# Kernel optimization log

Measured on AMD Instinct MI355X. Metric: run time of the kernel, lower is better.

The kernel has to match this reference:

```python
import jax, jax.numpy as jnp
import numpy as np

N_VOCAB = 50257
N_EMBED = 300
N_HIDDEN = 256
N_OUTPUT = 1
BATCH = 256
SEQ_LEN = 512


def setup_inputs() -> dict:
    key = jax.random.key(0)
    k1, k2, k3, k4, k5, k6 = jax.random.split(key, 6)
    input_words = jax.random.randint(k1, (BATCH, SEQ_LEN), 0, N_VOCAB, dtype=jnp.int64 if jax.config.jax_enable_x64 else jnp.int32)
    emb_table = jax.random.normal(k2, (N_VOCAB, N_EMBED), dtype=jnp.float32)
    Wi = jax.random.normal(k3, (N_EMBED, N_HIDDEN), dtype=jnp.float32)
    Wh = jax.random.normal(k4, (N_HIDDEN, N_HIDDEN), dtype=jnp.float32)
    # nn.Linear default init: U(-1/sqrt(in), 1/sqrt(in))
    bound = 1.0 / np.sqrt(N_HIDDEN)
    fc_w = jax.random.uniform(k5, (N_HIDDEN, N_OUTPUT), minval=-bound, maxval=bound, dtype=jnp.float32)
    fc_b = jax.random.uniform(k6, (N_OUTPUT,), minval=-bound, maxval=bound, dtype=jnp.float32)
    return {"input_words": input_words, "emb_table": emb_table, "Wi": Wi, "Wh": Wh, "fc_w": fc_w, "fc_b": fc_b}


def reference(input_words, emb_table, Wi, Wh, fc_w, fc_b):
    # [B, S, E] -> [S, B, E] (module permutes to time-major)
    embedded = emb_table[input_words].transpose(1, 0, 2)
    h0 = jnp.zeros((input_words.shape[0], Wh.shape[0]), dtype=embedded.dtype)

    def step(h, x_t):
        # recurrence: h = sigmoid(x_t @ Wi + h @ Wh)
        h_new = jax.nn.sigmoid(x_t @ Wi + h @ Wh)
        return h_new, None

    hidden, _ = jax.lax.scan(step, h0, embedded)
    sig = jax.nn.sigmoid(hidden @ fc_w + fc_b)
    return (sig, hidden)
```

## Files before the change

kernel.cpp:

```cpp
#include <hip/hip_runtime.h>

#define S_LEN 512
#define BATCH 256
#define EMB   300
#define HID   256
#define VOCAB 50257
#define NPROD 786
#define NLOG2E -1.44269504089f

#define EW_BYTES 25731584ull
#define KPAD 320

typedef __attribute__((ext_vector_type(8))) _Float16 f16x8;
typedef __attribute__((ext_vector_type(4))) _Float16 f16x4;
typedef __attribute__((ext_vector_type(2))) __fp16   fp16v2;
typedef __attribute__((ext_vector_type(4))) float    f32x4;

__device__ __forceinline__ void block_sync_lds() {
    asm volatile("" ::: "memory");
    __builtin_amdgcn_s_waitcnt(0xC07F);
    __builtin_amdgcn_s_barrier();
    asm volatile("" ::: "memory");
}

__device__ __forceinline__ float sigmoid_scaled(float xs) {
    float e = __builtin_amdgcn_exp2f(xs);
    return __builtin_amdgcn_rcpf(1.0f + e);
}

__global__ __launch_bounds__(256)
void k_wprep(const float* __restrict__ Wi, _Float16* __restrict__ WiT) {
    const int k = blockIdx.x;
    const int n = threadIdx.x;
    _Float16 v = (_Float16)0.f;
    if (k < EMB) v = (_Float16)(Wi[k * HID + n] * NLOG2E);
    WiT[n * KPAD + k] = v;
}

__global__ __launch_bounds__(256, 3)
void k_embwi(const float* __restrict__ emb, const _Float16* __restrict__ WiT,
             _Float16* __restrict__ EW) {
    const int tid  = threadIdx.x;
    const int wv   = tid >> 6;
    const int lane = tid & 63;
    const int ln   = lane & 15;
    const int q    = lane >> 4;
    const int m0   = blockIdx.x * 64;

    const _Float16* wbn[4];
#pragma unroll
    for (int nt = 0; nt < 4; nt++)
        wbn[nt] = WiT + (wv * 64 + nt * 16 + ln) * KPAD + q * 8;

    const float* arow[4];
#pragma unroll
    for (int mt = 0; mt < 4; mt++) {
        int row = m0 + mt * 16 + ln; if (row >= VOCAB) row = VOCAB - 1;
        arow[mt] = emb + (long)row * EMB + q * 8;
    }

    auto load_af = [&](int kc, int mt) -> f16x8 {
        const float* p = arow[mt] + kc * 32;
        f16x8 v;
        if (kc < 9 || q == 0) {
            f32x4 a = *(const f32x4*)p;
            f32x4 b = *(const f32x4*)(p + 4);
#pragma unroll
            for (int r = 0; r < 4; r++) { v[r] = (_Float16)a[r]; v[4 + r] = (_Float16)b[r]; }
        } else if (q == 1) {
            f32x4 a = *(const f32x4*)p;
#pragma unroll
            for (int r = 0; r < 4; r++) { v[r] = (_Float16)a[r]; v[4 + r] = (_Float16)0.f; }
        } else {
#pragma unroll
            for (int r = 0; r < 8; r++) v[r] = (_Float16)0.f;
        }
        return v;
    };

    f32x4 acc[4][4];
#pragma unroll
    for (int mt = 0; mt < 4; mt++)
#pragma unroll
        for (int nt = 0; nt < 4; nt++)
            acc[mt][nt] = f32x4{0.f, 0.f, 0.f, 0.f};

#pragma unroll
    for (int kc = 0; kc < 10; kc++) {
        f16x8 af[4], bf[4];
#pragma unroll
        for (int mt = 0; mt < 4; mt++) af[mt] = load_af(kc, mt);
#pragma unroll
        for (int nt = 0; nt < 4; nt++) bf[nt] = *(const f16x8*)(wbn[nt] + kc * 32);
#pragma unroll
        for (int mt = 0; mt < 4; mt++)
#pragma unroll
            for (int nt = 0; nt < 4; nt++)
                acc[mt][nt] = __builtin_amdgcn_mfma_f32_16x16x32_f16(
                    af[mt], bf[nt], acc[mt][nt], 0, 0, 0);
    }

#pragma unroll
    for (int mt = 0; mt < 4; mt++)
#pragma unroll
        for (int nt = 0; nt < 4; nt++) {
            const int col = wv * 64 + nt * 16 + ln;
#pragma unroll
            for (int r = 0; r < 4; r++) {
                const int mm = m0 + mt * 16 + q * 4 + r;
                if (mm < VOCAB) EW[(long)mm * HID + col] = (_Float16)acc[mt][nt][r];
            }
        }
}

#define HSTR 272
#define HB8  (8 * HSTR)
#define WSTR 513

__global__ __launch_bounds__(512, 2)
void k_recur(const float* __restrict__ Wh, const _Float16* __restrict__ EW,
             const int* __restrict__ words,
             const float* __restrict__ fcw, const float* __restrict__ fcb,
             float* __restrict__ out) {
    __shared__ __attribute__((aligned(16))) _Float16 hbuf[2 * HB8];
    __shared__ float red[512];
    __shared__ int   wlds[8 * WSTR];

    const int tid  = threadIdx.x;
    const int wv   = tid >> 6;
    const int lane = tid & 63;
    const int ln   = lane & 15;
    const int lnn  = ln & 7;
    const int q    = lane >> 4;
    const int b0   = blockIdx.x * 8;

    f16x8 whf[8][2];
#pragma unroll
    for (int kc = 0; kc < 8; kc++) {
#pragma unroll
        for (int mt = 0; mt < 2; mt++) {
            const int j = wv * 32 + mt * 16 + ln;
            f16x8 u;
#pragma unroll
            for (int jj = 0; jj < 8; jj++)
                u[jj] = (_Float16)(Wh[(kc * 32 + q * 8 + jj) * HID + j] * NLOG2E);
            whf[kc][mt] = u;
        }
    }

#pragma unroll
    for (int i = tid; i < 8 * S_LEN; i += 512) {
        const int r = i >> 9, c = i & 511;
        wlds[r * WSTR + c] = words[(b0 + r) * S_LEN + c];
    }
    for (int i = tid; i < 2 * HB8; i += 512) hbuf[i] = (_Float16)0.f;
    __syncthreads();

    const int jbase = wv * 32 + q * 4;
    f16x4 abuf0[2], abuf1[2];
    {
        const int w0 = wlds[lnn * WSTR + 0];
        const int w1 = wlds[lnn * WSTR + 1];
        const _Float16* p0 = EW + ((long)w0 << 8) + jbase;
        const _Float16* p1 = EW + ((long)w1 << 8) + jbase;
#pragma unroll
        for (int mt = 0; mt < 2; mt++) abuf0[mt] = *(const f16x4*)(p0 + mt * 16);
#pragma unroll
        for (int mt = 0; mt < 2; mt++) abuf1[mt] = *(const f16x4*)(p1 + mt * 16);
    }

#define STEP(T, ABUF)                                                                   \
    {                                                                                   \
        const int tt = (T);                                                             \
        const _Float16* hr = hbuf + ((tt & 1) ? HB8 : 0);                               \
        _Float16*       hw = hbuf + ((tt & 1) ? 0 : HB8);                               \
        f16x8 hf[8];                                                                    \
        _Pragma("unroll")                                                               \
        for (int kc = 0; kc < 8; kc++)                                                  \
            hf[kc] = *(const f16x8*)(hr + lnn * HSTR + kc * 32 + q * 8);                \
        f32x4 acc_a[2], acc_b[2];                                                       \
        _Pragma("unroll")                                                               \
        for (int mt = 0; mt < 2; mt++) {               \
            f16x4 av = ABUF[mt];                                                        \
            acc_a[mt] = f32x4{(float)av[0], (float)av[1], (float)av[2], (float)av[3]};  \
            acc_b[mt] = f32x4{0.f, 0.f, 0.f, 0.f};                                      \
        }                                                                               \
        const int t2 = (tt + 2 > 511) ? 511 : (tt + 2);                                 \
        const int wrow = wlds[lnn * WSTR + t2];                                         \
        const _Float16* rp = EW + ((long)wrow << 8) + jbase;                            \
        _Pragma("unroll")                                                               \
        for (int mt = 0; mt < 2; mt++) ABUF[mt] = *(const f16x4*)(rp + mt * 16);        \
        _Pragma("unroll")                                                               \
        for (int r = 0; r < 4; r++) {                            \
            _Pragma("unroll")                                                           \
            for (int mt = 0; mt < 2; mt++)                                              \
                acc_a[mt] = __builtin_amdgcn_mfma_f32_16x16x32_f16(                     \
                    whf[r][mt], hf[r], acc_a[mt], 0, 0, 0);                             \
            _Pragma("unroll")                                                           \
            for (int mt = 0; mt < 2; mt++)                                              \
                acc_b[mt] = __builtin_amdgcn_mfma_f32_16x16x32_f16(                     \
                    whf[r + 4][mt], hf[r + 4], acc_b[mt], 0, 0, 0);                     \
        }                                                                               \
        _Pragma("unroll")                                                               \
        for (int mt = 0; mt < 2; mt++) {                                                \
            f32x4 s = acc_a[mt] + acc_b[mt];                                            \
            float r0 = sigmoid_scaled(s[0]), r1 = sigmoid_scaled(s[1]);                 \
            float r2 = sigmoid_scaled(s[2]), r3 = sigmoid_scaled(s[3]);                 \
            union { fp16v2 h2[2]; f16x4 v4; } hp;                                       \
            hp.h2[0] = __builtin_amdgcn_cvt_pkrtz(r0, r1);                              \
            hp.h2[1] = __builtin_amdgcn_cvt_pkrtz(r2, r3);                              \
            if (ln < 8)                                                                 \
                *(f16x4*)(hw + ln * HSTR + wv * 32 + mt * 16 + q * 4) = hp.v4;          \
        }                                                                               \
        block_sync_lds();                                                               \
    }

    for (int t = 0; t < S_LEN; t += 2) {
        STEP(t, abuf0);
        STEP(t + 1, abuf1);
    }
#undef STEP

    const _Float16* hf0 = hbuf;

    {
        const int row = tid >> 6, j0 = (tid & 63) * 4;
        float* dst = out + 256 + (long)(b0 + row) * HID + j0;
        f32x4 w;
#pragma unroll
        for (int r = 0; r < 4; r++) w[r] = (float)hf0[row * HSTR + j0 + r];
        *(f32x4*)dst = w;
    }

    {
        const int row = tid >> 6, part = tid & 63;
        float s = 0.f;
#pragma unroll
        for (int jj = 0; jj < 4; jj++) {
            const int j = part * 4 + jj;
            s += (float)hf0[row * HSTR + j] * fcw[j];
        }
        red[row * 64 + part] = s;
    }
    __syncthreads();
    if (tid < 8) {
        float s = fcb[0];
#pragma unroll
        for (int p = 0; p < 64; p++) s += red[tid * 64 + p];
        s *= NLOG2E;
        out[b0 + tid] = sigmoid_scaled(s);
    }
}

extern "C" void kernel_launch(void* const* d_in, const int* in_sizes, int n_in,
                              void* d_out, int out_size, void* d_ws, size_t ws_size,
                              hipStream_t stream) {
    const int*   words = (const int*)d_in[0];
    const float* emb   = (const float*)d_in[1];
    const float* Wi    = (const float*)d_in[2];
    const float* Wh    = (const float*)d_in[3];
    const float* fcw   = (const float*)d_in[4];
    const float* fcb   = (const float*)d_in[5];
    _Float16* EW   = (_Float16*)d_ws;
    _Float16* WiT  = (_Float16*)((char*)d_ws + EW_BYTES);
    float*    outp = (float*)d_out;

    hipLaunchKernelGGL(k_wprep, dim3(KPAD), dim3(256), 0, stream, Wi, WiT);
    hipLaunchKernelGGL(k_embwi, dim3(NPROD), dim3(256), 0, stream, emb, WiT, EW);
    hipLaunchKernelGGL(k_recur, dim3(BATCH / 8), dim3(512), 0, stream,
                       Wh, EW, words, fcw, fcb, outp);
}
```

Measured before the change: 419.0 us.

## Interleave two independent batch groups per block in the recurrence

Each recurrence block now handles 16 batch rows as two independent 8-row groups with separate hidden-state buffers. It alternates between them so that one group's LDS read of the hidden state overlaps the other group's MFMA and sigmoid work, hiding per-step latency in the serial chain. The grid is halved to 16 blocks and the launch bound drops to 1 block per SM. This trades parallelism across CUs for latency hiding within each block, and raises register and LDS pressure.

```diff
diff --git a/kernel.cpp b/kernel.cpp
--- a/kernel.cpp
+++ b/kernel.cpp
@@ -117,14 +117,15 @@
 #define HB8  (8 * HSTR)
 #define WSTR 513
 
-__global__ __launch_bounds__(512, 2)
+__global__ __launch_bounds__(512, 1)
 void k_recur(const float* __restrict__ Wh, const _Float16* __restrict__ EW,
              const int* __restrict__ words,
              const float* __restrict__ fcw, const float* __restrict__ fcb,
              float* __restrict__ out) {
-    __shared__ __attribute__((aligned(16))) _Float16 hbuf[2 * HB8];
+    __shared__ __attribute__((aligned(16))) _Float16 hbufA[2 * HB8];
+    __shared__ __attribute__((aligned(16))) _Float16 hbufB[2 * HB8];
     __shared__ float red[512];
-    __shared__ int   wlds[8 * WSTR];
+    __shared__ int   wlds[16 * WSTR];
 
     const int tid  = threadIdx.x;
     const int wv   = tid >> 6;
@@ -132,7 +133,7 @@
     const int ln   = lane & 15;
     const int lnn  = ln & 7;
     const int q    = lane >> 4;
-    const int b0   = blockIdx.x * 8;
+    const int b0   = blockIdx.x * 16;
 
     f16x8 whf[8][2];
 #pragma unroll
@@ -149,57 +150,60 @@
     }
 
 #pragma unroll
-    for (int i = tid; i < 8 * S_LEN; i += 512) {
+    for (int i = tid; i < 16 * S_LEN; i += 512) {
         const int r = i >> 9, c = i & 511;
         wlds[r * WSTR + c] = words[(b0 + r) * S_LEN + c];
     }
-    for (int i = tid; i < 2 * HB8; i += 512) hbuf[i] = (_Float16)0.f;
+    for (int i = tid; i < 2 * HB8; i += 512) { hbufA[i] = (_Float16)0.f; hbufB[i] = (_Float16)0.f; }
     __syncthreads();
 
     const int jbase = wv * 32 + q * 4;
-    f16x4 abuf0[2], abuf1[2];
+    const int* wrA = wlds + lnn * WSTR;
+    const int* wrB = wlds + (8 + lnn) * WSTR;
+
+    f16x4 abA0[2], abA1[2], abB0[2], abB1[2];
     {
-        const int w0 = wlds[lnn * WSTR + 0];
-        const int w1 = wlds[lnn * WSTR + 1];
-        const _Float16* p0 = EW + ((long)w0 << 8) + jbase;
-        const _Float16* p1 = EW + ((long)w1 << 8) + jbase;
-#pragma unroll
-        for (int mt = 0; mt < 2; mt++) abuf0[mt] = *(const f16x4*)(p0 + mt * 16);
-#pragma unroll
-        for (int mt = 0; mt < 2; mt++) abuf1[mt] = *(const f16x4*)(p1 + mt * 16);
-    }
-
-#define STEP(T, ABUF)                                                                   \
+        const _Float16* pA0 = EW + ((long)wrA[0] << 8) + jbase;
+        const _Float16* pA1 = EW + ((long)wrA[1] << 8) + jbase;
+        const _Float16* pB0 = EW + ((long)wrB[0] << 8) + jbase;
+        const _Float16* pB1 = EW + ((long)wrB[1] << 8) + jbase;
+#pragma unroll
+        for (int mt = 0; mt < 2; mt++) {
+            abA0[mt] = *(const f16x4*)(pA0 + mt * 16);
+            abA1[mt] = *(const f16x4*)(pA1 + mt * 16);
+            abB0[mt] = *(const f16x4*)(pB0 + mt * 16);
+            abB1[mt] = *(const f16x4*)(pB1 + mt * 16);
+        }
+    }
+
+#define READH(HF, HR)                                                                   \
+    _Pragma("unroll")                                                                   \
+    for (int kc = 0; kc < 8; kc++)                                                      \
+        HF[kc] = *(const f16x8*)((HR) + lnn * HSTR + kc * 32 + q * 8);
+
+#define GCOMP(HF, AB, HW, WR, T)                                                        \
     {                                                                                   \
-        const int tt = (T);                                                             \
-        const _Float16* hr = hbuf + ((tt & 1) ? HB8 : 0);                               \
-        _Float16*       hw = hbuf + ((tt & 1) ? 0 : HB8);                               \
-        f16x8 hf[8];                                                                    \
-        _Pragma("unroll")                                                               \
-        for (int kc = 0; kc < 8; kc++)                                                  \
-            hf[kc] = *(const f16x8*)(hr + lnn * HSTR + kc * 32 + q * 8);                \
         f32x4 acc_a[2], acc_b[2];                                                       \
         _Pragma("unroll")                                                               \
         for (int mt = 0; mt < 2; mt++) {               \
-            f16x4 av = ABUF[mt];                                                        \
+            f16x4 av = AB[mt];                                                          \
             acc_a[mt] = f32x4{(float)av[0], (float)av[1], (float)av[2], (float)av[3]};  \
             acc_b[mt] = f32x4{0.f, 0.f, 0.f, 0.f};                                      \
         }                                                                               \
-        const int t2 = (tt + 2 > 511) ? 511 : (tt + 2);                                 \
-        const int wrow = wlds[lnn * WSTR + t2];                                         \
-        const _Float16* rp = EW + ((long)wrow << 8) + jbase;                            \
-        _Pragma("unroll")                                                               \
-        for (int mt = 0; mt < 2; mt++) ABUF[mt] = *(const f16x4*)(rp + mt * 16);        \
+        const int t2_ = ((T) + 2 > 511) ? 511 : ((T) + 2);                              \
+        const _Float16* rp_ = EW + ((long)WR[t2_] << 8) + jbase;                        \
+        _Pragma("unroll")                                                               \
+        for (int mt = 0; mt < 2; mt++) AB[mt] = *(const f16x4*)(rp_ + mt * 16);         \
         _Pragma("unroll")                                                               \
         for (int r = 0; r < 4; r++) {                            \
             _Pragma("unroll")                                                           \
             for (int mt = 0; mt < 2; mt++)                                              \
                 acc_a[mt] = __builtin_amdgcn_mfma_f32_16x16x32_f16(                     \
-                    whf[r][mt], hf[r], acc_a[mt], 0, 0, 0);                             \
+                    whf[r][mt], HF[r], acc_a[mt], 0, 0, 0);                             \
             _Pragma("unroll")                                                           \
             for (int mt = 0; mt < 2; mt++)                                              \
                 acc_b[mt] = __builtin_amdgcn_mfma_f32_16x16x32_f16(                     \
-                    whf[r + 4][mt], hf[r + 4], acc_b[mt], 0, 0, 0);                     \
+                    whf[r + 4][mt], HF[r + 4], acc_b[mt], 0, 0, 0);                     \
         }                                                                               \
         _Pragma("unroll")                                                               \
         for (int mt = 0; mt < 2; mt++) {                                                \
@@ -210,43 +214,63 @@
             hp.h2[0] = __builtin_amdgcn_cvt_pkrtz(r0, r1);                              \
             hp.h2[1] = __builtin_amdgcn_cvt_pkrtz(r2, r3);                              \
             if (ln < 8)                                                                 \
-                *(f16x4*)(hw + ln * HSTR + wv * 32 + mt * 16 + q * 4) = hp.v4;          \
+                *(f16x4*)((HW) + ln * HSTR + wv * 32 + mt * 16 + q * 4) = hp.v4;        \
         }                                                                               \
+    }
+
+#define PHASE(T, ABA, ABB, HRB, HWA, HWB)                                               \
+    {                                                                                   \
+        READH(hfB, HRB);                                                                \
+        GCOMP(hfA, ABA, HWA, wrA, T);                                                   \
         block_sync_lds();                                                               \
-    }
+        READH(hfA, HWA);                                                                \
+        GCOMP(hfB, ABB, HWB, wrB, T);                                                   \
+        block_sync_lds();                                                               \
+    }
+
+    f16x8 hfA[8], hfB[8];
+    READH(hfA, hbufA);
 
     for (int t = 0; t < S_LEN; t += 2) {
-        STEP(t, abuf0);
-        STEP(t + 1, abuf1);
-    }
-#undef STEP
-
-    const _Float16* hf0 = hbuf;
+        PHASE(t,     abA0, abB0, hbufB,       hbufA + HB8, hbufB + HB8);
+        PHASE(t + 1, abA1, abB1, hbufB + HB8, hbufA,       hbufB);
+    }
+#undef PHASE
+#undef GCOMP
+#undef READH
 
     {
-        const int row = tid >> 6, j0 = (tid & 63) * 4;
+        const int row = tid >> 5, j0 = (tid & 31) * 8;
+        const _Float16* hsrc = (row < 8) ? (hbufA + row * HSTR)
+                                         : (hbufB + (row - 8) * HSTR);
         float* dst = out + 256 + (long)(b0 + row) * HID + j0;
-        f32x4 w;
-#pragma unroll
-        for (int r = 0; r < 4; r++) w[r] = (float)hf0[row * HSTR + j0 + r];
-        *(f32x4*)dst = w;
+        f32x4 w0v, w1v;
+#pragma unroll
+        for (int r = 0; r < 4; r++) {
+            w0v[r] = (float)hsrc[j0 + r];
+            w1v[r] = (float)hsrc[j0 + 4 + r];
+        }
+        *(f32x4*)dst = w0v;
+        *(f32x4*)(dst + 4) = w1v;
     }
 
     {
-        const int row = tid >> 6, part = tid & 63;
+        const int row = tid >> 5, part = tid & 31;
+        const _Float16* hsrc = (row < 8) ? (hbufA + row * HSTR)
+                                         : (hbufB + (row - 8) * HSTR);
         float s = 0.f;
 #pragma unroll
-        for (int jj = 0; jj < 4; jj++) {
-            const int j = part * 4 + jj;
-            s += (float)hf0[row * HSTR + j] * fcw[j];
-        }
-        red[row * 64 + part] = s;
+        for (int jj = 0; jj < 8; jj++) {
+            const int j = part * 8 + jj;
+            s += (float)hsrc[j] * fcw[j];
+        }
+        red[row * 32 + part] = s;
     }
     __syncthreads();
-    if (tid < 8) {
+    if (tid < 16) {
         float s = fcb[0];
 #pragma unroll
-        for (int p = 0; p < 64; p++) s += red[tid * 64 + p];
+        for (int p = 0; p < 32; p++) s += red[tid * 32 + p];
         s *= NLOG2E;
         out[b0 + tid] = sigmoid_scaled(s);
     }
@@ -267,6 +291,6 @@
 
     hipLaunchKernelGGL(k_wprep, dim3(KPAD), dim3(256), 0, stream, Wi, WiT);
     hipLaunchKernelGGL(k_embwi, dim3(NPROD), dim3(256), 0, stream, emb, WiT, EW);
-    hipLaunchKernelGGL(k_recur, dim3(BATCH / 8), dim3(512), 0, stream,
+    hipLaunchKernelGGL(k_recur, dim3(BATCH / 16), dim3(512), 0, stream,
                        Wh, EW, words, fcw, fcb, outp);
 }
```

New measurement: 659.0 us. +57.3%, slower.

## Split recurrence across more blocks with two batch rows each and four accumulator chains

Applied to the files above, without the earlier changes.

Each block now handles 2 batch rows instead of 8, so the recurrence kernel launches 128 blocks instead of 32 and uses more of the GPU's compute units. The MFMA chain is split into four independent accumulators so dependent MFMA latency can overlap. The cost is that most of each 16-wide MFMA tile is wasted on duplicated rows, and Wh is loaded into registers by four times as many blocks.

```diff
diff --git a/kernel.cpp b/kernel.cpp
--- a/kernel.cpp
+++ b/kernel.cpp
@@ -114,7 +114,8 @@
 }
 
 #define HSTR 272
-#define HB8  (8 * HSTR)
+#define NR   2
+#define HBR  (NR * HSTR)
 #define WSTR 513
 
 __global__ __launch_bounds__(512, 2)
@@ -122,17 +123,17 @@
              const int* __restrict__ words,
              const float* __restrict__ fcw, const float* __restrict__ fcb,
              float* __restrict__ out) {
-    __shared__ __attribute__((aligned(16))) _Float16 hbuf[2 * HB8];
-    __shared__ float red[512];
-    __shared__ int   wlds[8 * WSTR];
+    __shared__ __attribute__((aligned(16))) _Float16 hbuf[2 * HBR];
+    __shared__ float red[128];
+    __shared__ int   wlds[NR * WSTR];
 
     const int tid  = threadIdx.x;
     const int wv   = tid >> 6;
     const int lane = tid & 63;
     const int ln   = lane & 15;
-    const int lnn  = ln & 7;
+    const int lnn  = ln & (NR - 1);
     const int q    = lane >> 4;
-    const int b0   = blockIdx.x * 8;
+    const int b0   = blockIdx.x * NR;
 
     f16x8 whf[8][2];
 #pragma unroll
@@ -148,12 +149,11 @@
         }
     }
 
-#pragma unroll
-    for (int i = tid; i < 8 * S_LEN; i += 512) {
+    for (int i = tid; i < NR * S_LEN; i += 512) {
         const int r = i >> 9, c = i & 511;
         wlds[r * WSTR + c] = words[(b0 + r) * S_LEN + c];
     }
-    for (int i = tid; i < 2 * HB8; i += 512) hbuf[i] = (_Float16)0.f;
+    for (int i = tid; i < 2 * HBR; i += 512) hbuf[i] = (_Float16)0.f;
     __syncthreads();
 
     const int jbase = wv * 32 + q * 4;
@@ -172,18 +172,20 @@
 #define STEP(T, ABUF)                                                                   \
     {                                                                                   \
         const int tt = (T);                                                             \
-        const _Float16* hr = hbuf + ((tt & 1) ? HB8 : 0);                               \
-        _Float16*       hw = hbuf + ((tt & 1) ? 0 : HB8);                               \
+        const _Float16* hr = hbuf + ((tt & 1) ? HBR : 0);                               \
+        _Float16*       hw = hbuf + ((tt & 1) ? 0 : HBR);                               \
         f16x8 hf[8];                                                                    \
         _Pragma("unroll")                                                               \
         for (int kc = 0; kc < 8; kc++)                                                  \
             hf[kc] = *(const f16x8*)(hr + lnn * HSTR + kc * 32 + q * 8);                \
-        f32x4 acc_a[2], acc_b[2];                                                       \
+        f32x4 c0[2], c1[2], c2[2], c3[2];                                               \
         _Pragma("unroll")                                                               \
         for (int mt = 0; mt < 2; mt++) {               \
             f16x4 av = ABUF[mt];                                                        \
-            acc_a[mt] = f32x4{(float)av[0], (float)av[1], (float)av[2], (float)av[3]};  \
-            acc_b[mt] = f32x4{0.f, 0.f, 0.f, 0.f};                                      \
+            c0[mt] = f32x4{(float)av[0], (float)av[1], (float)av[2], (float)av[3]};     \
+            c1[mt] = f32x4{0.f, 0.f, 0.f, 0.f};                                         \
+            c2[mt] = f32x4{0.f, 0.f, 0.f, 0.f};                                         \
+            c3[mt] = f32x4{0.f, 0.f, 0.f, 0.f};                                         \
         }                                                                               \
         const int t2 = (tt + 2 > 511) ? 511 : (tt + 2);                                 \
         const int wrow = wlds[lnn * WSTR + t2];                                         \
@@ -191,26 +193,27 @@
         _Pragma("unroll")                                                               \
         for (int mt = 0; mt < 2; mt++) ABUF[mt] = *(const f16x4*)(rp + mt * 16);        \
         _Pragma("unroll")                                                               \
-        for (int r = 0; r < 4; r++) {                            \
+        for (int mt = 0; mt < 2; mt++) {                         \
+            c0[mt] = __builtin_amdgcn_mfma_f32_16x16x32_f16(whf[0][mt], hf[0], c0[mt], 0, 0, 0); \
+            c1[mt] = __builtin_amdgcn_mfma_f32_16x16x32_f16(whf[2][mt], hf[2], c1[mt], 0, 0, 0); \
+            c2[mt] = __builtin_amdgcn_mfma_f32_16x16x32_f16(whf[4][mt], hf[4], c2[mt], 0, 0, 0); \
+            c3[mt] = __builtin_amdgcn_mfma_f32_16x16x32_f16(whf[6][mt], hf[6], c3[mt], 0, 0, 0); \
+            c0[mt] = __builtin_amdgcn_mfma_f32_16x16x32_f16(whf[1][mt], hf[1], c0[mt], 0, 0, 0); \
+            c1[mt] = __builtin_amdgcn_mfma_f32_16x16x32_f16(whf[3][mt], hf[3], c1[mt], 0, 0, 0); \
+            c2[mt] = __builtin_amdgcn_mfma_f32_16x16x32_f16(whf[5][mt], hf[5], c2[mt], 0, 0, 0); \
+            c3[mt] = __builtin_amdgcn_mfma_f32_16x16x32_f16(whf[7][mt], hf[7], c3[mt], 0, 0, 0); \
+        }                                                                               \
+        if (ln < NR) {                                   \
             _Pragma("unroll")                                                           \
-            for (int mt = 0; mt < 2; mt++)                                              \
-                acc_a[mt] = __builtin_amdgcn_mfma_f32_16x16x32_f16(                     \
-                    whf[r][mt], hf[r], acc_a[mt], 0, 0, 0);                             \
-            _Pragma("unroll")                                                           \
-            for (int mt = 0; mt < 2; mt++)                                              \
-                acc_b[mt] = __builtin_amdgcn_mfma_f32_16x16x32_f16(                     \
-                    whf[r + 4][mt], hf[r + 4], acc_b[mt], 0, 0, 0);                     \
-        }                                                                               \
-        _Pragma("unroll")                                                               \
-        for (int mt = 0; mt < 2; mt++) {                                                \
-            f32x4 s = acc_a[mt] + acc_b[mt];                                            \
-            float r0 = sigmoid_scaled(s[0]), r1 = sigmoid_scaled(s[1]);                 \
-            float r2 = sigmoid_scaled(s[2]), r3 = sigmoid_scaled(s[3]);                 \
-            union { fp16v2 h2[2]; f16x4 v4; } hp;                                       \
-            hp.h2[0] = __builtin_amdgcn_cvt_pkrtz(r0, r1);                              \
-            hp.h2[1] = __builtin_amdgcn_cvt_pkrtz(r2, r3);                              \
-            if (ln < 8)                                                                 \
+            for (int mt = 0; mt < 2; mt++) {                                            \
+                f32x4 s = (c0[mt] + c1[mt]) + (c2[mt] + c3[mt]);                        \
+                float r0 = sigmoid_scaled(s[0]), r1 = sigmoid_scaled(s[1]);             \
+                float r2 = sigmoid_scaled(s[2]), r3 = sigmoid_scaled(s[3]);             \
+                union { fp16v2 h2[2]; f16x4 v4; } hp;                                   \
+                hp.h2[0] = __builtin_amdgcn_cvt_pkrtz(r0, r1);                          \
+                hp.h2[1] = __builtin_amdgcn_cvt_pkrtz(r2, r3);                          \
                 *(f16x4*)(hw + ln * HSTR + wv * 32 + mt * 16 + q * 4) = hp.v4;          \
+            }                                                                           \
         }                                                                               \
         block_sync_lds();                                                               \
     }
@@ -223,7 +226,7 @@
 
     const _Float16* hf0 = hbuf;
 
-    {
+    if (tid < 64 * NR) {
         const int row = tid >> 6, j0 = (tid & 63) * 4;
         float* dst = out + 256 + (long)(b0 + row) * HID + j0;
         f32x4 w;
@@ -232,7 +235,7 @@
         *(f32x4*)dst = w;
     }
 
-    {
+    if (tid < 64 * NR) {
         const int row = tid >> 6, part = tid & 63;
         float s = 0.f;
 #pragma unroll
@@ -243,7 +246,7 @@
         red[row * 64 + part] = s;
     }
     __syncthreads();
-    if (tid < 8) {
+    if (tid < NR) {
         float s = fcb[0];
 #pragma unroll
         for (int p = 0; p < 64; p++) s += red[tid * 64 + p];
@@ -267,6 +270,6 @@
 
     hipLaunchKernelGGL(k_wprep, dim3(KPAD), dim3(256), 0, stream, Wi, WiT);
     hipLaunchKernelGGL(k_embwi, dim3(NPROD), dim3(256), 0, stream, emb, WiT, EW);
-    hipLaunchKernelGGL(k_recur, dim3(BATCH / 8), dim3(512), 0, stream,
+    hipLaunchKernelGGL(k_recur, dim3(BATCH / NR), dim3(512), 0, stream,
                        Wh, EW, words, fcw, fcb, outp);
 }
```

Result: slower. 439.2 us (+4.8%).

## Permute EW columns for single 16-byte gather and drop split accumulators

Applied to the files above, without the earlier changes.

The projection kernel now writes EW with a permuted column order within each 32-column group. This lets each lane in the recurrence load its input contribution with one 8-half vector load per step instead of two 4-half loads. The recurrence uses two accumulators over all 8 k-chunks instead of four split ones. Lanes 8-15 take the second m-tile's result, so all 16 lanes do the sigmoid and store, which removes the masked half-idle epilogue. The last two steps are peeled so the clamp on the prefetch index no longer runs inside the loop. The trade-off is a longer dependent MFMA chain per accumulator in exchange for fewer adds and loads.

```diff
diff --git a/kernel.cpp b/kernel.cpp
--- a/kernel.cpp
+++ b/kernel.cpp
@@ -105,10 +105,12 @@
 #pragma unroll
         for (int nt = 0; nt < 4; nt++) {
             const int col = wv * 64 + nt * 16 + ln;
+            const int low = col & 31;
+            const int colp = (col & ~31) | (((low >> 2) & 3) << 3) | ((low >> 4) << 2) | (low & 3);
 #pragma unroll
             for (int r = 0; r < 4; r++) {
                 const int mm = m0 + mt * 16 + q * 4 + r;
-                if (mm < VOCAB) EW[(long)mm * HID + col] = (_Float16)acc[mt][nt][r];
+                if (mm < VOCAB) EW[(long)mm * HID + colp] = (_Float16)acc[mt][nt][r];
             }
         }
 }
@@ -133,6 +135,7 @@
     const int lnn  = ln & 7;
     const int q    = lane >> 4;
     const int b0   = blockIdx.x * 8;
+    const int half = (ln >= 8) ? 1 : 0;
 
     f16x8 whf[8][2];
 #pragma unroll
@@ -156,20 +159,16 @@
     for (int i = tid; i < 2 * HB8; i += 512) hbuf[i] = (_Float16)0.f;
     __syncthreads();
 
-    const int jbase = wv * 32 + q * 4;
-    f16x4 abuf0[2], abuf1[2];
+    const int jb8 = wv * 32 + q * 8;
+    f16x8 abuf0, abuf1;
     {
         const int w0 = wlds[lnn * WSTR + 0];
         const int w1 = wlds[lnn * WSTR + 1];
-        const _Float16* p0 = EW + ((long)w0 << 8) + jbase;
-        const _Float16* p1 = EW + ((long)w1 << 8) + jbase;
-#pragma unroll
-        for (int mt = 0; mt < 2; mt++) abuf0[mt] = *(const f16x4*)(p0 + mt * 16);
-#pragma unroll
-        for (int mt = 0; mt < 2; mt++) abuf1[mt] = *(const f16x4*)(p1 + mt * 16);
-    }
-
-#define STEP(T, ABUF)                                                                   \
+        abuf0 = *(const f16x8*)(EW + ((long)w0 << 8) + jb8);
+        abuf1 = *(const f16x8*)(EW + ((long)w1 << 8) + jb8);
+    }
+
+#define STEP(T, ABUF, T2)                                                               \
     {                                                                                   \
         const int tt = (T);                                                             \
         const _Float16* hr = hbuf + ((tt & 1) ? HB8 : 0);                               \
@@ -178,47 +177,37 @@
         _Pragma("unroll")                                                               \
         for (int kc = 0; kc < 8; kc++)                                                  \
             hf[kc] = *(const f16x8*)(hr + lnn * HSTR + kc * 32 + q * 8);                \
-        f32x4 acc_a[2], acc_b[2];                                                       \
+        f32x4 acc0, acc1;                              \
+        acc0 = f32x4{(float)ABUF[0], (float)ABUF[1], (float)ABUF[2], (float)ABUF[3]};   \
+        acc1 = f32x4{(float)ABUF[4], (float)ABUF[5], (float)ABUF[6], (float)ABUF[7]};   \
+        const int wrow = wlds[lnn * WSTR + (T2)];                                       \
+        ABUF = *(const f16x8*)(EW + ((long)wrow << 8) + jb8);                           \
         _Pragma("unroll")                                                               \
-        for (int mt = 0; mt < 2; mt++) {               \
-            f16x4 av = ABUF[mt];                                                        \
-            acc_a[mt] = f32x4{(float)av[0], (float)av[1], (float)av[2], (float)av[3]};  \
-            acc_b[mt] = f32x4{0.f, 0.f, 0.f, 0.f};                                      \
+        for (int r = 0; r < 8; r++) {                            \
+            acc0 = __builtin_amdgcn_mfma_f32_16x16x32_f16(whf[r][0], hf[r], acc0, 0, 0, 0); \
+            acc1 = __builtin_amdgcn_mfma_f32_16x16x32_f16(whf[r][1], hf[r], acc1, 0, 0, 0); \
         }                                                                               \
-        const int t2 = (tt + 2 > 511) ? 511 : (tt + 2);                                 \
-        const int wrow = wlds[lnn * WSTR + t2];                                         \
-        const _Float16* rp = EW + ((long)wrow << 8) + jbase;                            \
-        _Pragma("unroll")                                                               \
-        for (int mt = 0; mt < 2; mt++) ABUF[mt] = *(const f16x4*)(rp + mt * 16);        \
-        _Pragma("unroll")                                                               \
-        for (int r = 0; r < 4; r++) {                            \
-            _Pragma("unroll")                                                           \
-            for (int mt = 0; mt < 2; mt++)                                              \
-                acc_a[mt] = __builtin_amdgcn_mfma_f32_16x16x32_f16(                     \
-                    whf[r][mt], hf[r], acc_a[mt], 0, 0, 0);                             \
-            _Pragma("unroll")                                                           \
-            for (int mt = 0; mt < 2; mt++)                                              \
-                acc_b[mt] = __builtin_amdgcn_mfma_f32_16x16x32_f16(                     \
-                    whf[r + 4][mt], hf[r + 4], acc_b[mt], 0, 0, 0);                     \
-        }                                                                               \
-        _Pragma("unroll")                                                               \
-        for (int mt = 0; mt < 2; mt++) {                                                \
-            f32x4 s = acc_a[mt] + acc_b[mt];                                            \
-            float r0 = sigmoid_scaled(s[0]), r1 = sigmoid_scaled(s[1]);                 \
-            float r2 = sigmoid_scaled(s[2]), r3 = sigmoid_scaled(s[3]);                 \
+        {            \
+            float s0 = half ? acc1[0] : acc0[0];                                        \
+            float s1 = half ? acc1[1] : acc0[1];                                        \
+            float s2 = half ? acc1[2] : acc0[2];                                        \
+            float s3 = half ? acc1[3] : acc0[3];                                        \
+            float r0 = sigmoid_scaled(s0), r1 = sigmoid_scaled(s1);                     \
+            float r2 = sigmoid_scaled(s2), r3 = sigmoid_scaled(s3);                     \
             union { fp16v2 h2[2]; f16x4 v4; } hp;                                       \
             hp.h2[0] = __builtin_amdgcn_cvt_pkrtz(r0, r1);                              \
             hp.h2[1] = __builtin_amdgcn_cvt_pkrtz(r2, r3);                              \
-            if (ln < 8)                                                                 \
-                *(f16x4*)(hw + ln * HSTR + wv * 32 + mt * 16 + q * 4) = hp.v4;          \
+            *(f16x4*)(hw + lnn * HSTR + wv * 32 + half * 16 + q * 4) = hp.v4;           \
         }                                                                               \
         block_sync_lds();                                                               \
     }
 
-    for (int t = 0; t < S_LEN; t += 2) {
-        STEP(t, abuf0);
-        STEP(t + 1, abuf1);
-    }
+    for (int t = 0; t < 510; t += 2) {
+        STEP(t, abuf0, tt + 2);
+        STEP(t + 1, abuf1, tt + 2);
+    }
+    STEP(510, abuf0, 511);
+    STEP(511, abuf1, 511);
 #undef STEP
 
     const _Float16* hf0 = hbuf;
```

Result: faster. 397.1 us (-5.2%).
